# Kernel optimization log

Measured on AMD Instinct MI355X. Metric: run time of the kernel, lower is better.

Reference implementation:

```python
import jax, jax.numpy as jnp
import numpy as np

N_NODES = 100000
E_MAIN = 1600000   # '_E' edges
E_ACC = 200000     # 'account' edges
D = 128            # dim_in == dim_out
FE = 4             # edge feature width (hard-coded in source)


def setup_inputs() -> dict:
    key = jax.random.key(0)
    ks = jax.random.split(key, 14)
    inp = {
        "feats": jax.random.normal(ks[0], (N_NODES, D), jnp.float32),
        "edge_feats": jax.random.normal(ks[1], (E_MAIN, FE), jnp.float32),
        "src_E": jax.random.randint(ks[2], (E_MAIN,), 0, N_NODES),
        "dst_E": jax.random.randint(ks[3], (E_MAIN,), 0, N_NODES),
        "src_acc": jax.random.randint(ks[4], (E_ACC,), 0, N_NODES),
        "dst_acc": jax.random.randint(ks[5], (E_ACC,), 0, N_NODES),
        "W_skip": jax.random.normal(ks[6], (D, D), jnp.float32) * 0.05,
        "b_skip": jnp.zeros((D,), jnp.float32),
        "W_msg": jax.random.normal(ks[7], (D, D), jnp.float32) * 0.05,
        "b_msg": jnp.zeros((D,), jnp.float32),
        "W_edge": jax.random.normal(ks[8], (D, FE), jnp.float32) * 0.5,
        "b_edge": jax.random.normal(ks[9], (D,), jnp.float32) * 0.1,
        "W_att": jax.random.normal(ks[10], (1, FE), jnp.float32) * 0.5,
        "b_att": jax.random.normal(ks[11], (1,), jnp.float32) * 0.1,
    }
    return inp


def reference(feats, edge_feats, src_E, dst_E, src_acc, dst_acc,
              W_skip, b_skip, W_msg, b_msg, W_edge, b_edge, W_att, b_att):
    n = feats.shape[0]
    # symmetric-ish degree norm from '_E' source rows (matches self.norm)
    deg = jax.ops.segment_sum(jnp.ones(src_E.shape[0], feats.dtype), src_E,
                              num_segments=n)
    deg_safe = jnp.where(deg > 0, deg, 1.0)
    norm = jnp.where(deg > 0, deg_safe ** -0.5, 0.0)  # [N]
    h = feats * norm[:, None]                         # srcdata['h'] == dstdata['h']

    def messages(ef, s, d):
        # per-edge: sigmoid attention * src + transformed edge feat + dst
        att = jax.nn.sigmoid(ef @ W_att.T + b_att)    # [E,1]
        tr = ef @ W_edge.T + b_edge                   # [E,D]
        return att * h[s] + tr + h[d]                 # [E,D]

    agg = jax.ops.segment_sum(messages(edge_feats, src_E, dst_E), dst_E,
                              num_segments=n)
    # 'account' etype gets zero edge features (as in source)
    ef_acc = jnp.zeros((src_acc.shape[0], edge_feats.shape[1]), feats.dtype)
    agg = agg + jax.ops.segment_sum(messages(ef_acc, src_acc, dst_acc), dst_acc,
                                    num_segments=n)

    rst = agg * norm[:, None]
    return rst @ W_msg.T + b_msg + (feats @ W_skip.T + b_skip)
```

## Files before the change

### kernel.cpp

```cpp
#include <hip/hip_runtime.h>
#include <hip/hip_bf16.h>

#define NN 100000
#define NP 100096
#define EM 1600000
#define EA 200000
#define ET (EM + EA)
#define SB 98

#define HC 128
#define CNT_CHUNK 14063
#define DEG_CHUNK 12500
#define PITCHW 25024
#define PITCHB 100096

#define OFF_NORM 0
#define OFF_CNT  (NN)
#define OFF_CUR  (2*NN)
#define OFF_BSUM (3*NN)
#define OFF_WB   (3*NN + 128)
#define OFF_RSC  (OFF_WB + 16384)
#define OFF_REF  (OFF_RSC + ET)
#define OFF_FB   (OFF_REF + 2*ET)
#define OFF_RB   (OFF_FB + 64*NP)
#define OFF_RANK (OFF_RB + 64*NP)

#define UNP_LO(u) __uint_as_float((u) << 16)
#define UNP_HI(u) __uint_as_float((u) & 0xFFFF0000u)

typedef __attribute__((ext_vector_type(8))) short bf16x8;
typedef __attribute__((ext_vector_type(4))) float f32x4;

static __device__ __forceinline__ unsigned pack_bf16x2(float a, float b) {
  union { __hip_bfloat162 v; unsigned u; } cv;
  cv.v = __float22bfloat162_rn(make_float2(a, b));
  return cv.u;
}

__global__ __launch_bounds__(256) void k_convert(
    const float* __restrict__ feats, unsigned* __restrict__ featsb) {
  int i = blockIdx.x * 256 + threadIdx.x;
  if (i >= NP * 64) return;
  if (i < NN * 64) {
    float2 f = ((const float2*)feats)[i];
    featsb[i] = pack_bf16x2(f.x, f.y);
  } else {
    featsb[i] = 0u;
  }
}

__global__ __launch_bounds__(1024) void k_hist(
    const int* __restrict__ srcE, const int* __restrict__ dstE,
    const int* __restrict__ dstA,
    unsigned* __restrict__ hist8w, unsigned* __restrict__ deg8w,
    unsigned short* __restrict__ rank16) {
  __shared__ unsigned h[PITCHW];
  int tid = threadIdx.x;
  for (int i = tid; i < PITCHW; i += 1024) h[i] = 0u;
  __syncthreads();
  int bid = blockIdx.x;
  if (bid < HC) {
    int c = bid;
    int e1 = c * CNT_CHUNK + CNT_CHUNK; if (e1 > ET) e1 = ET;
    for (int e = c * CNT_CHUNK + tid; e < e1; e += 1024) {
      int d = (e < EM) ? dstE[e] : dstA[e - EM];
      unsigned sh = 8u * (unsigned)(d & 3);
      unsigned old = atomicAdd(&h[d >> 2], 1u << sh);
      unsigned lr = (old >> sh) & 255u;
      rank16[e] = (unsigned short)(((unsigned)c << 9) | lr);
    }
    __syncthreads();
    unsigned* dst = hist8w + (size_t)c * PITCHW;
    for (int i = tid; i < PITCHW; i += 1024) dst[i] = h[i];
  } else {
    int c = bid - HC;
    int e1 = c * DEG_CHUNK + DEG_CHUNK;
    for (int e = c * DEG_CHUNK + tid; e < e1; e += 1024) {
      int s = srcE[e];
      atomicAdd(&h[s >> 2], 1u << (8u * (unsigned)(s & 3)));
    }
    __syncthreads();
    unsigned* dst = deg8w + (size_t)c * PITCHW;
    for (int i = tid; i < PITCHW; i += 1024) dst[i] = h[i];
  }
}

__global__ __launch_bounds__(256) void k_merge_wt(
    unsigned char* __restrict__ hist8, const unsigned char* __restrict__ deg8,
    unsigned* __restrict__ cnt, float* __restrict__ norm,
    const float* __restrict__ Wmsg, const float* __restrict__ Wskip,
    unsigned* __restrict__ Wb) {
  int i = blockIdx.x * 256 + threadIdx.x;
  if (i < NN) {
    unsigned t = 0;
    for (int c = 0; c < HC; ++c) {
      unsigned char* p = hist8 + (size_t)c * PITCHB + i;
      unsigned b = *p;
      *p = (unsigned char)t;
      t += b;
    }
    cnt[i] = t;
    unsigned dg = 0;
    for (int c = 0; c < HC; ++c) dg += deg8[(size_t)c * PITCHB + i];
    norm[i] = dg ? rsqrtf((float)dg) : 0.0f;
  }
  if (i < 16384) {
    int j = i >> 7, kk = i & 127;
    float a, b;
    if (kk < 64) {
      a = Wmsg[j * 128 + 2 * kk];
      b = Wmsg[j * 128 + 2 * kk + 1];
    } else {
      a = Wskip[j * 128 + 2 * kk - 128];
      b = Wskip[j * 128 + 2 * kk - 127];
    }
    Wb[j * 128 + kk] = pack_bf16x2(a, b);
  }
}

__global__ __launch_bounds__(1024) void k_scan1(const unsigned* __restrict__ cnt,
                                                int* __restrict__ bsum) {
  __shared__ int ws16[16];
  int tid = threadIdx.x, lane = tid & 63, wid = tid >> 6;
  int i = blockIdx.x * 1024 + tid;
  int v = (i < NN) ? (int)cnt[i] : 0;
#pragma unroll
  for (int s = 1; s < 64; s <<= 1) v += __shfl_xor(v, s, 64);
  if (lane == 0) ws16[wid] = v;
  __syncthreads();
  if (tid == 0) {
    int a = 0;
#pragma unroll
    for (int w = 0; w < 16; ++w) a += ws16[w];
    bsum[blockIdx.x] = a;
  }
}

__global__ __launch_bounds__(64) void k_scan2(int* __restrict__ bsum) {
  int lane = threadIdx.x;
  int v0 = (lane < SB) ? bsum[lane] : 0;
  int v1 = (64 + lane < SB) ? bsum[64 + lane] : 0;
  int x0 = v0, x1 = v1;
#pragma unroll
  for (int s = 1; s < 64; s <<= 1) {
    int y = __shfl_up(x0, s, 64); if (lane >= s) x0 += y;
  }
#pragma unroll
  for (int s = 1; s < 64; s <<= 1) {
    int y = __shfl_up(x1, s, 64); if (lane >= s) x1 += y;
  }
  int t0 = __shfl(x0, 63, 64);
  if (lane < SB) bsum[lane] = x0 - v0;
  if (64 + lane < SB) bsum[64 + lane] = t0 + x1 - v1;
}

__global__ __launch_bounds__(1024) void k_scan3(const unsigned* __restrict__ cnt,
                                                const int* __restrict__ bsum,
                                                int* __restrict__ cursor) {
  __shared__ int ws16[16];
  int tid = threadIdx.x, lane = tid & 63, wid = tid >> 6;
  int i = blockIdx.x * 1024 + tid;
  int v = (i < NN) ? (int)cnt[i] : 0;
  int x = v;
#pragma unroll
  for (int s = 1; s < 64; s <<= 1) {
    int y = __shfl_up(x, s, 64); if (lane >= s) x += y;
  }
  if (lane == 63) ws16[wid] = x;
  __syncthreads();
  if (tid == 0) {
    int a = bsum[blockIdx.x];
#pragma unroll
    for (int w = 0; w < 16; ++w) { int t = ws16[w]; ws16[w] = a; a += t; }
  }
  __syncthreads();
  if (i < NN) cursor[i] = ws16[wid] + x - v;
}

__global__ __launch_bounds__(256) void k_fill(
    const int* __restrict__ srcE, const int* __restrict__ dstE,
    const int* __restrict__ srcA, const int* __restrict__ dstA,
    const float* __restrict__ ef, const float* __restrict__ Watt,
    const float* __restrict__ batt, const float* __restrict__ norm,
    const int* __restrict__ cursor, const unsigned char* __restrict__ hist8,
    const unsigned short* __restrict__ rank16,
    unsigned* __restrict__ recSC, uint2* __restrict__ recEF) {
  int e = blockIdx.x * 256 + threadIdx.x;
  if (e >= ET) return;
  int s, d;
  float att;
  float4 f;
  if (e < EM) {
    s = srcE[e]; d = dstE[e];
    f = ((const float4*)ef)[e];
    float z = f.x * Watt[0] + f.y * Watt[1] + f.z * Watt[2] + f.w * Watt[3] + batt[0];
    att = 1.0f / (1.0f + __expf(-z));
  } else {
    int ea = e - EM;
    s = srcA[ea]; d = dstA[ea];
    f = make_float4(0.f, 0.f, 0.f, 0.f);
    att = 1.0f / (1.0f + __expf(-batt[0]));
  }
  float c = att * norm[s];
  unsigned q = (unsigned)(c * 32767.0f + 0.5f);
  if (q > 32767u) q = 32767u;
  unsigned rr = rank16[e];
  int slot = cursor[d] + (int)hist8[(size_t)(rr >> 9) * PITCHB + d]
           + (int)(rr & 511u);
  recSC[slot] = ((unsigned)s << 15) | q;
  recEF[slot] = make_uint2(pack_bf16x2(f.x, f.y), pack_bf16x2(f.z, f.w));
}

__global__ __launch_bounds__(256) void k_pull(
    const float* __restrict__ feats, const unsigned* __restrict__ featsb,
    const unsigned* __restrict__ cnt, const int* __restrict__ cursor,
    const float* __restrict__ norm, const unsigned* __restrict__ recSC,
    const uint2* __restrict__ recEF,
    const float* __restrict__ Wedge, const float* __restrict__ bedge,
    unsigned* __restrict__ rstb) {
  int lane = threadIdx.x & 63, wid = threadIdx.x >> 6;
  int n = blockIdx.x * 4 + wid;
  if (n >= NP) return;
  if (n >= NN) { rstb[n * 64 + lane] = 0u; return; }

  int beg = __builtin_amdgcn_readfirstlane(cursor[n]);
  int len = __builtin_amdgcn_readfirstlane((int)cnt[n]);
  int end = beg + len;
  float2 acc = make_float2(0.f, 0.f);
  int e = beg;
  for (; e + 8 <= end; e += 8) {
    unsigned r0 = recSC[e+0], r1 = recSC[e+1], r2 = recSC[e+2], r3 = recSC[e+3];
    unsigned r4 = recSC[e+4], r5 = recSC[e+5], r6 = recSC[e+6], r7 = recSC[e+7];
    unsigned u0 = featsb[(r0 >> 15) * 64 + lane];
    unsigned u1 = featsb[(r1 >> 15) * 64 + lane];
    unsigned u2 = featsb[(r2 >> 15) * 64 + lane];
    unsigned u3 = featsb[(r3 >> 15) * 64 + lane];
    unsigned u4 = featsb[(r4 >> 15) * 64 + lane];
    unsigned u5 = featsb[(r5 >> 15) * 64 + lane];
    unsigned u6 = featsb[(r6 >> 15) * 64 + lane];
    unsigned u7 = featsb[(r7 >> 15) * 64 + lane];
    float c0 = (float)(r0 & 32767u) * (1.0f / 32767.0f);
    float c1 = (float)(r1 & 32767u) * (1.0f / 32767.0f);
    float c2 = (float)(r2 & 32767u) * (1.0f / 32767.0f);
    float c3 = (float)(r3 & 32767u) * (1.0f / 32767.0f);
    float c4 = (float)(r4 & 32767u) * (1.0f / 32767.0f);
    float c5 = (float)(r5 & 32767u) * (1.0f / 32767.0f);
    float c6 = (float)(r6 & 32767u) * (1.0f / 32767.0f);
    float c7 = (float)(r7 & 32767u) * (1.0f / 32767.0f);
    acc.x += c0 * UNP_LO(u0) + c1 * UNP_LO(u1) + c2 * UNP_LO(u2) + c3 * UNP_LO(u3)
           + c4 * UNP_LO(u4) + c5 * UNP_LO(u5) + c6 * UNP_LO(u6) + c7 * UNP_LO(u7);
    acc.y += c0 * UNP_HI(u0) + c1 * UNP_HI(u1) + c2 * UNP_HI(u2) + c3 * UNP_HI(u3)
           + c4 * UNP_HI(u4) + c5 * UNP_HI(u5) + c6 * UNP_HI(u6) + c7 * UNP_HI(u7);
  }
  for (; e < end; ++e) {
    unsigned r = recSC[e];
    unsigned u = featsb[(r >> 15) * 64 + lane];
    float c = (float)(r & 32767u) * (1.0f / 32767.0f);
    acc.x += c * UNP_LO(u);
    acc.y += c * UNP_HI(u);
  }
  float4 efa = make_float4(0.f, 0.f, 0.f, 0.f);
  for (int b = beg + lane; b < end; b += 64) {
    uint2 g = recEF[b];
    efa.x += UNP_LO(g.x); efa.y += UNP_HI(g.x);
    efa.z += UNP_LO(g.y); efa.w += UNP_HI(g.y);
  }
#pragma unroll
  for (int s = 1; s < 64; s <<= 1) {
    efa.x += __shfl_xor(efa.x, s, 64);
    efa.y += __shfl_xor(efa.y, s, 64);
    efa.z += __shfl_xor(efa.z, s, 64);
    efa.w += __shfl_xor(efa.w, s, 64);
  }
  float flen = (float)len;
  float nm = norm[n];
  float2 f = ((const float2*)feats)[n * 64 + lane];
  float4 wa = ((const float4*)Wedge)[2 * lane + 0];
  float4 wb = ((const float4*)Wedge)[2 * lane + 1];
  float2 be = ((const float2*)bedge)[lane];
  float tx = wa.x * efa.x + wa.y * efa.y + wa.z * efa.z + wa.w * efa.w;
  float ty = wb.x * efa.x + wb.y * efa.y + wb.z * efa.z + wb.w * efa.w;
  float rx = (acc.x + tx + flen * (be.x + nm * f.x)) * nm;
  float ry = (acc.y + ty + flen * (be.y + nm * f.y)) * nm;
  rstb[n * 64 + lane] = pack_bf16x2(rx, ry);
}

__global__ __launch_bounds__(256) void k_gemm(
    const unsigned* __restrict__ rstb, const unsigned* __restrict__ featsb,
    const unsigned* __restrict__ Wb,
    const float* __restrict__ bmsg, const float* __restrict__ bskip,
    float* __restrict__ out) {
  int lane = threadIdx.x & 63, wid = threadIdx.x >> 6;
  int quad = lane >> 4, l15 = lane & 15;
  int rowt = blockIdx.x * 128 + wid * 32;
  int m0 = rowt + l15;
  int m1 = m0 + 16;

  f32x4 acc0[8], acc1[8];
#pragma unroll
  for (int ct = 0; ct < 8; ++ct) {
    acc0[ct] = (f32x4){0.f, 0.f, 0.f, 0.f};
    acc1[ct] = (f32x4){0.f, 0.f, 0.f, 0.f};
  }

#pragma unroll
  for (int ks = 0; ks < 8; ++ks) {
    int kb = ks * 32;
    const unsigned* Xsrc = (kb < 128) ? rstb : featsb;
    int off = ((kb & 127) >> 1) + quad * 4;
    bf16x8 a0 = *(const bf16x8*)(Xsrc + m0 * 64 + off);
    bf16x8 a1 = *(const bf16x8*)(Xsrc + m1 * 64 + off);
#pragma unroll
    for (int ct = 0; ct < 8; ++ct) {
      int j = ct * 16 + l15;
      bf16x8 b = *(const bf16x8*)(Wb + j * 128 + (kb >> 1) + quad * 4);
      acc0[ct] = __builtin_amdgcn_mfma_f32_16x16x32_bf16(a0, b, acc0[ct], 0, 0, 0);
      acc1[ct] = __builtin_amdgcn_mfma_f32_16x16x32_bf16(a1, b, acc1[ct], 0, 0, 0);
    }
  }

#pragma unroll
  for (int ct = 0; ct < 8; ++ct) {
    int col = ct * 16 + l15;
    float bia = bmsg[col] + bskip[col];
#pragma unroll
    for (int r = 0; r < 4; ++r) {
      int row0 = rowt + quad * 4 + r;
      if (row0 < NN) out[row0 * 128 + col] = acc0[ct][r] + bia;
      int row1 = row0 + 16;
      if (row1 < NN) out[row1 * 128 + col] = acc1[ct][r] + bia;
    }
  }
}

extern "C" void kernel_launch(void* const* d_in, const int* in_sizes, int n_in,
                              void* d_out, int out_size, void* d_ws, size_t ws_size,
                              hipStream_t stream) {
  const float* feats  = (const float*)d_in[0];
  const float* ef     = (const float*)d_in[1];
  const int*   srcE   = (const int*)d_in[2];
  const int*   dstE   = (const int*)d_in[3];
  const int*   srcA   = (const int*)d_in[4];
  const int*   dstA   = (const int*)d_in[5];
  const float* Wskip  = (const float*)d_in[6];
  const float* bskip  = (const float*)d_in[7];
  const float* Wmsg   = (const float*)d_in[8];
  const float* bmsg   = (const float*)d_in[9];
  const float* Wedge  = (const float*)d_in[10];
  const float* bedge  = (const float*)d_in[11];
  const float* Watt   = (const float*)d_in[12];
  const float* batt   = (const float*)d_in[13];
  float* out = (float*)d_out;
  float* ws  = (float*)d_ws;

  float*          norm   = ws + OFF_NORM;
  unsigned*       cnt    = (unsigned*)(ws + OFF_CNT);
  int*            cursor = (int*)(ws + OFF_CUR);
  int*            bsum   = (int*)(ws + OFF_BSUM);
  unsigned*       Wb     = (unsigned*)(ws + OFF_WB);
  unsigned*       recSC  = (unsigned*)(ws + OFF_RSC);
  uint2*          recEF  = (uint2*)(ws + OFF_REF);
  unsigned*       featsb = (unsigned*)(ws + OFF_FB);
  unsigned*       rstb   = (unsigned*)(ws + OFF_RB);
  unsigned short* rank16 = (unsigned short*)(ws + OFF_RANK);

  unsigned*       hist8w = rstb;
  unsigned*       deg8w  = rstb + (size_t)HC * PITCHW;
  unsigned char*  hist8b = (unsigned char*)hist8w;
  unsigned char*  deg8b  = (unsigned char*)deg8w;

  k_convert<<<(NP * 64 + 255) / 256, 256, 0, stream>>>(feats, featsb);
  k_hist<<<2 * HC, 1024, 0, stream>>>(srcE, dstE, dstA, hist8w, deg8w, rank16);
  k_merge_wt<<<(NN + 255) / 256, 256, 0, stream>>>(hist8b, deg8b, cnt, norm,
                                                   Wmsg, Wskip, Wb);
  k_scan1<<<SB, 1024, 0, stream>>>(cnt, bsum);
  k_scan2<<<1, 64, 0, stream>>>(bsum);
  k_scan3<<<SB, 1024, 0, stream>>>(cnt, bsum, cursor);
  k_fill<<<(ET + 255) / 256, 256, 0, stream>>>(srcE, dstE, srcA, dstA, ef, Watt,
                                               batt, norm, cursor, hist8b,
                                               rank16, recSC, recEF);
  k_pull<<<NP / 4, 256, 0, stream>>>(feats, featsb, cnt, cursor, norm,
                                     recSC, recEF, Wedge, bedge, rstb);
  k_gemm<<<NP / 128, 256, 0, stream>>>(rstb, featsb, Wb, bmsg, bskip, out);
}
```

Before: 397.3 us.

## Pack edge records into 16-byte struct and fold bf16 conversion into histogram kernel

Merges the separate 4-byte src/coef and 8-byte edge-feature record arrays into a single 16-byte record holding the full source index, fp32 coefficient and packed bf16 edge features. The pull kernel now accumulates edge features inside the main gather loop, which removes the separate strided pass and the cross-lane shuffle reduction. The coefficient is also no longer quantized to 15 bits. The feature bf16 conversion kernel is folded into the histogram kernel to save a launch. The cost is a larger record footprint, 16 bytes per edge instead of 12, written scattered in the fill kernel.

```diff
diff --git a/kernel.cpp b/kernel.cpp
--- a/kernel.cpp
+++ b/kernel.cpp
@@ -19,9 +19,8 @@
 #define OFF_CUR  (2*NN)
 #define OFF_BSUM (3*NN)
 #define OFF_WB   (3*NN + 128)
-#define OFF_RSC  (OFF_WB + 16384)
-#define OFF_REF  (OFF_RSC + ET)
-#define OFF_FB   (OFF_REF + 2*ET)
+#define OFF_REC  (OFF_WB + 16384)
+#define OFF_FB   (OFF_REC + 4*ET)
 #define OFF_RB   (OFF_FB + 64*NP)
 #define OFF_RANK (OFF_RB + 64*NP)
 
@@ -37,28 +36,27 @@
   return cv.u;
 }
 
-__global__ __launch_bounds__(256) void k_convert(
-    const float* __restrict__ feats, unsigned* __restrict__ featsb) {
-  int i = blockIdx.x * 256 + threadIdx.x;
-  if (i >= NP * 64) return;
-  if (i < NN * 64) {
-    float2 f = ((const float2*)feats)[i];
-    featsb[i] = pack_bf16x2(f.x, f.y);
-  } else {
-    featsb[i] = 0u;
-  }
-}
-
 __global__ __launch_bounds__(1024) void k_hist(
     const int* __restrict__ srcE, const int* __restrict__ dstE,
-    const int* __restrict__ dstA,
+    const int* __restrict__ dstA, const float* __restrict__ feats,
+    unsigned* __restrict__ featsb,
     unsigned* __restrict__ hist8w, unsigned* __restrict__ deg8w,
     unsigned short* __restrict__ rank16) {
   __shared__ unsigned h[PITCHW];
   int tid = threadIdx.x;
+  int bid = blockIdx.x;
+
+  for (int i = bid * 1024 + tid; i < NP * 64; i += 2 * HC * 1024) {
+    if (i < NN * 64) {
+      float2 f = ((const float2*)feats)[i];
+      featsb[i] = pack_bf16x2(f.x, f.y);
+    } else {
+      featsb[i] = 0u;
+    }
+  }
+
   for (int i = tid; i < PITCHW; i += 1024) h[i] = 0u;
   __syncthreads();
-  int bid = blockIdx.x;
   if (bid < HC) {
     int c = bid;
     int e1 = c * CNT_CHUNK + CNT_CHUNK; if (e1 > ET) e1 = ET;
@@ -184,7 +182,7 @@
     const float* __restrict__ batt, const float* __restrict__ norm,
     const int* __restrict__ cursor, const unsigned char* __restrict__ hist8,
     const unsigned short* __restrict__ rank16,
-    unsigned* __restrict__ recSC, uint2* __restrict__ recEF) {
+    uint4* __restrict__ rec) {
   int e = blockIdx.x * 256 + threadIdx.x;
   if (e >= ET) return;
   int s, d;
@@ -202,20 +200,17 @@
     att = 1.0f / (1.0f + __expf(-batt[0]));
   }
   float c = att * norm[s];
-  unsigned q = (unsigned)(c * 32767.0f + 0.5f);
-  if (q > 32767u) q = 32767u;
   unsigned rr = rank16[e];
   int slot = cursor[d] + (int)hist8[(size_t)(rr >> 9) * PITCHB + d]
            + (int)(rr & 511u);
-  recSC[slot] = ((unsigned)s << 15) | q;
-  recEF[slot] = make_uint2(pack_bf16x2(f.x, f.y), pack_bf16x2(f.z, f.w));
+  rec[slot] = make_uint4((unsigned)s, __float_as_uint(c),
+                         pack_bf16x2(f.x, f.y), pack_bf16x2(f.z, f.w));
 }
 
 __global__ __launch_bounds__(256) void k_pull(
     const float* __restrict__ feats, const unsigned* __restrict__ featsb,
     const unsigned* __restrict__ cnt, const int* __restrict__ cursor,
-    const float* __restrict__ norm, const unsigned* __restrict__ recSC,
-    const uint2* __restrict__ recEF,
+    const float* __restrict__ norm, const uint4* __restrict__ rec,
     const float* __restrict__ Wedge, const float* __restrict__ bedge,
     unsigned* __restrict__ rstb) {
   int lane = threadIdx.x & 63, wid = threadIdx.x >> 6;
@@ -227,50 +222,44 @@
   int len = __builtin_amdgcn_readfirstlane((int)cnt[n]);
   int end = beg + len;
   float2 acc = make_float2(0.f, 0.f);
+  float4 efa = make_float4(0.f, 0.f, 0.f, 0.f);
   int e = beg;
   for (; e + 8 <= end; e += 8) {
-    unsigned r0 = recSC[e+0], r1 = recSC[e+1], r2 = recSC[e+2], r3 = recSC[e+3];
-    unsigned r4 = recSC[e+4], r5 = recSC[e+5], r6 = recSC[e+6], r7 = recSC[e+7];
-    unsigned u0 = featsb[(r0 >> 15) * 64 + lane];
-    unsigned u1 = featsb[(r1 >> 15) * 64 + lane];
-    unsigned u2 = featsb[(r2 >> 15) * 64 + lane];
-    unsigned u3 = featsb[(r3 >> 15) * 64 + lane];
-    unsigned u4 = featsb[(r4 >> 15) * 64 + lane];
-    unsigned u5 = featsb[(r5 >> 15) * 64 + lane];
-    unsigned u6 = featsb[(r6 >> 15) * 64 + lane];
-    unsigned u7 = featsb[(r7 >> 15) * 64 + lane];
-    float c0 = (float)(r0 & 32767u) * (1.0f / 32767.0f);
-    float c1 = (float)(r1 & 32767u) * (1.0f / 32767.0f);
-    float c2 = (float)(r2 & 32767u) * (1.0f / 32767.0f);
-    float c3 = (float)(r3 & 32767u) * (1.0f / 32767.0f);
-    float c4 = (float)(r4 & 32767u) * (1.0f / 32767.0f);
-    float c5 = (float)(r5 & 32767u) * (1.0f / 32767.0f);
-    float c6 = (float)(r6 & 32767u) * (1.0f / 32767.0f);
-    float c7 = (float)(r7 & 32767u) * (1.0f / 32767.0f);
+    uint4 r0 = rec[e+0], r1 = rec[e+1], r2 = rec[e+2], r3 = rec[e+3];
+    uint4 r4 = rec[e+4], r5 = rec[e+5], r6 = rec[e+6], r7 = rec[e+7];
+    unsigned u0 = featsb[r0.x * 64 + lane];
+    unsigned u1 = featsb[r1.x * 64 + lane];
+    unsigned u2 = featsb[r2.x * 64 + lane];
+    unsigned u3 = featsb[r3.x * 64 + lane];
+    unsigned u4 = featsb[r4.x * 64 + lane];
+    unsigned u5 = featsb[r5.x * 64 + lane];
+    unsigned u6 = featsb[r6.x * 64 + lane];
+    unsigned u7 = featsb[r7.x * 64 + lane];
+    float c0 = __uint_as_float(r0.y), c1 = __uint_as_float(r1.y);
+    float c2 = __uint_as_float(r2.y), c3 = __uint_as_float(r3.y);
+    float c4 = __uint_as_float(r4.y), c5 = __uint_as_float(r5.y);
+    float c6 = __uint_as_float(r6.y), c7 = __uint_as_float(r7.y);
     acc.x += c0 * UNP_LO(u0) + c1 * UNP_LO(u1) + c2 * UNP_LO(u2) + c3 * UNP_LO(u3)
            + c4 * UNP_LO(u4) + c5 * UNP_LO(u5) + c6 * UNP_LO(u6) + c7 * UNP_LO(u7);
     acc.y += c0 * UNP_HI(u0) + c1 * UNP_HI(u1) + c2 * UNP_HI(u2) + c3 * UNP_HI(u3)
            + c4 * UNP_HI(u4) + c5 * UNP_HI(u5) + c6 * UNP_HI(u6) + c7 * UNP_HI(u7);
+    efa.x += UNP_LO(r0.z) + UNP_LO(r1.z) + UNP_LO(r2.z) + UNP_LO(r3.z)
+           + UNP_LO(r4.z) + UNP_LO(r5.z) + UNP_LO(r6.z) + UNP_LO(r7.z);
+    efa.y += UNP_HI(r0.z) + UNP_HI(r1.z) + UNP_HI(r2.z) + UNP_HI(r3.z)
+           + UNP_HI(r4.z) + UNP_HI(r5.z) + UNP_HI(r6.z) + UNP_HI(r7.z);
+    efa.z += UNP_LO(r0.w) + UNP_LO(r1.w) + UNP_LO(r2.w) + UNP_LO(r3.w)
+           + UNP_LO(r4.w) + UNP_LO(r5.w) + UNP_LO(r6.w) + UNP_LO(r7.w);
+    efa.w += UNP_HI(r0.w) + UNP_HI(r1.w) + UNP_HI(r2.w) + UNP_HI(r3.w)
+           + UNP_HI(r4.w) + UNP_HI(r5.w) + UNP_HI(r6.w) + UNP_HI(r7.w);
   }
   for (; e < end; ++e) {
-    unsigned r = recSC[e];
-    unsigned u = featsb[(r >> 15) * 64 + lane];
-    float c = (float)(r & 32767u) * (1.0f / 32767.0f);
+    uint4 r = rec[e];
+    unsigned u = featsb[r.x * 64 + lane];
+    float c = __uint_as_float(r.y);
     acc.x += c * UNP_LO(u);
     acc.y += c * UNP_HI(u);
-  }
-  float4 efa = make_float4(0.f, 0.f, 0.f, 0.f);
-  for (int b = beg + lane; b < end; b += 64) {
-    uint2 g = recEF[b];
-    efa.x += UNP_LO(g.x); efa.y += UNP_HI(g.x);
-    efa.z += UNP_LO(g.y); efa.w += UNP_HI(g.y);
-  }
-#pragma unroll
-  for (int s = 1; s < 64; s <<= 1) {
-    efa.x += __shfl_xor(efa.x, s, 64);
-    efa.y += __shfl_xor(efa.y, s, 64);
-    efa.z += __shfl_xor(efa.z, s, 64);
-    efa.w += __shfl_xor(efa.w, s, 64);
+    efa.x += UNP_LO(r.z); efa.y += UNP_HI(r.z);
+    efa.z += UNP_LO(r.w); efa.w += UNP_HI(r.w);
   }
   float flen = (float)len;
   float nm = norm[n];
@@ -358,8 +347,7 @@
   int*            cursor = (int*)(ws + OFF_CUR);
   int*            bsum   = (int*)(ws + OFF_BSUM);
   unsigned*       Wb     = (unsigned*)(ws + OFF_WB);
-  unsigned*       recSC  = (unsigned*)(ws + OFF_RSC);
-  uint2*          recEF  = (uint2*)(ws + OFF_REF);
+  uint4*          rec    = (uint4*)(ws + OFF_REC);
   unsigned*       featsb = (unsigned*)(ws + OFF_FB);
   unsigned*       rstb   = (unsigned*)(ws + OFF_RB);
   unsigned short* rank16 = (unsigned short*)(ws + OFF_RANK);
@@ -369,8 +357,8 @@
   unsigned char*  hist8b = (unsigned char*)hist8w;
   unsigned char*  deg8b  = (unsigned char*)deg8w;
 
-  k_convert<<<(NP * 64 + 255) / 256, 256, 0, stream>>>(feats, featsb);
-  k_hist<<<2 * HC, 1024, 0, stream>>>(srcE, dstE, dstA, hist8w, deg8w, rank16);
+  k_hist<<<2 * HC, 1024, 0, stream>>>(srcE, dstE, dstA, feats, featsb,
+                                      hist8w, deg8w, rank16);
   k_merge_wt<<<(NN + 255) / 256, 256, 0, stream>>>(hist8b, deg8b, cnt, norm,
                                                    Wmsg, Wskip, Wb);
   k_scan1<<<SB, 1024, 0, stream>>>(cnt, bsum);
@@ -378,8 +366,8 @@
   k_scan3<<<SB, 1024, 0, stream>>>(cnt, bsum, cursor);
   k_fill<<<(ET + 255) / 256, 256, 0, stream>>>(srcE, dstE, srcA, dstA, ef, Watt,
                                                batt, norm, cursor, hist8b,
-                                               rank16, recSC, recEF);
+                                               rank16, rec);
   k_pull<<<NP / 4, 256, 0, stream>>>(feats, featsb, cnt, cursor, norm,
-                                     recSC, recEF, Wedge, bedge, rstb);
+                                     rec, Wedge, bedge, rstb);
   k_gemm<<<NP / 128, 256, 0, stream>>>(rstb, featsb, Wb, bmsg, bskip, out);
 }
```

Result: faster. 374.4 us (-5.8%).
